# Kernel optimization log

Hardware: AMD Instinct MI355X
Metric: run time of the kernel (lower is better)

The kernel has to match this reference:

```python
import jax, jax.numpy as jnp
import numpy as np

B, S, D, A, E = 32, 2048, 512, 64, 64
EPS = 1e-5

def setup_inputs() -> dict:
    key = jax.random.key(0)
    ks = jax.random.split(key, 12)
    sc = 0.02
    return {
        "source_embedding": jax.random.normal(ks[0], (B, E), jnp.float32),
        "inputs": jax.random.normal(ks[1], (B, S, D), jnp.float32),
        "down_w_W": sc * jax.random.normal(ks[2], (E, A * D), jnp.float32),
        "down_w_b": jnp.zeros((A * D,), jnp.float32),
        "down_b_W": sc * jax.random.normal(ks[3], (E, A), jnp.float32),
        "down_b_b": jnp.zeros((A,), jnp.float32),
        "up_w_W": sc * jax.random.normal(ks[4], (E, D * A), jnp.float32),
        "up_w_b": jnp.zeros((D * A,), jnp.float32),
        "up_b_W": sc * jax.random.normal(ks[5], (E, D), jnp.float32),
        "up_b_b": jnp.zeros((D,), jnp.float32),
        "pre_w_W": sc * jax.random.normal(ks[6], (E, D), jnp.float32),
        "pre_w_b": jnp.ones((D,), jnp.float32),
        "pre_b_W": sc * jax.random.normal(ks[7], (E, D), jnp.float32),
        "pre_b_b": jnp.zeros((D,), jnp.float32),
        "post_w_W": sc * jax.random.normal(ks[8], (E, D), jnp.float32),
        "post_w_b": jnp.ones((D,), jnp.float32),
        "post_b_W": sc * jax.random.normal(ks[9], (E, D), jnp.float32),
        "post_b_b": jnp.zeros((D,), jnp.float32),
    }

def _cond_ln(x, w, b):
    # x: [B,S,D]; w,b: [B,D] -> per-sample affine layernorm over last dim
    mean = jnp.mean(x, axis=2, keepdims=True)
    var = jnp.mean((x - mean) ** 2, axis=2, keepdims=True) + EPS
    return (x - mean) / jnp.sqrt(var) * w[:, None, :] + b[:, None, :]

def reference(source_embedding, inputs,
              down_w_W, down_w_b, down_b_W, down_b_b,
              up_w_W, up_w_b, up_b_W, up_b_b,
              pre_w_W, pre_w_b, pre_b_W, pre_b_b,
              post_w_W, post_w_b, post_b_W, post_b_b):
    emb = source_embedding  # [B,E]
    # hypernet-generated per-sample adapter weights
    w_down = (emb @ down_w_W + down_w_b).reshape(B, A, D)  # [B,A,D]
    b_down = emb @ down_b_W + down_b_b                      # [B,A]
    w_up = (emb @ up_w_W + up_w_b).reshape(B, D, A)         # [B,D,A]
    b_up = emb @ up_b_W + up_b_b                            # [B,D]
    # conditional pre layernorm
    pre_w = emb @ pre_w_W + pre_w_b
    pre_b = emb @ pre_b_W + pre_b_b
    z = _cond_ln(inputs, pre_w, pre_b)
    # adapter: down-proj, relu, up-proj (matmul with weight.transpose(1,2))
    down = jnp.einsum('bsd,bad->bsa', z, w_down) + b_down[:, None, :]
    mid = jax.nn.relu(down)
    out = jnp.einsum('bsa,bda->bsd', mid, w_up) + b_up[:, None, :]
    # conditional post layernorm
    post_w = emb @ post_w_W + post_w_b
    post_b = emb @ post_b_W + post_b_b
    out = _cond_ln(out, post_w, post_b)
    return out + inputs
```

## Files before the change

kernel.cpp:

```cpp
#include <hip/hip_runtime.h>

#define NB 32
#define NS 2048
#define ND 512
#define NA 64
#define NE 64

typedef __bf16 bf16x8 __attribute__((ext_vector_type(8)));
typedef float f32x4 __attribute__((ext_vector_type(4)));

__device__ __forceinline__ unsigned short f2bf(float f) {
    union { float f; unsigned u; } v; v.f = f;
    unsigned r = (v.u + 0x7fffu + ((v.u >> 16) & 1u)) >> 16;
    return (unsigned short)r;
}
__device__ __forceinline__ unsigned pk(float a, float b) {
    return (unsigned)f2bf(a) | ((unsigned)f2bf(b) << 16);
}

#define BAR() do { asm volatile("s_waitcnt lgkmcnt(0)" ::: "memory"); \
                   __builtin_amdgcn_s_barrier(); } while (0)

__global__ __launch_bounds__(256) void hyper_vec(
    const float* __restrict__ emb,
    const float* __restrict__ pwW, const float* __restrict__ pwb,
    const float* __restrict__ pbW, const float* __restrict__ pbb,
    const float* __restrict__ powW, const float* __restrict__ powb,
    const float* __restrict__ pobW, const float* __restrict__ pobb,
    const float* __restrict__ ubW, const float* __restrict__ ubb,
    const float* __restrict__ dbW, const float* __restrict__ dbb,
    float* __restrict__ vecs) {
    int gid = blockIdx.x * 256 + threadIdx.x;
    if (gid >= NB * 2624) return;
    int b = gid / 2624;
    int r = gid - b * 2624;
    const float* W; const float* bias; int off, width;
    if (r < 2560) {
        int v = r >> 9; off = r & 511; width = 512;
        switch (v) {
            case 0:  W = pwW;  bias = pwb;  break;
            case 1:  W = pbW;  bias = pbb;  break;
            case 2:  W = powW; bias = powb; break;
            case 3:  W = pobW; bias = pobb; break;
            default: W = ubW;  bias = ubb;  break;
        }
    } else {
        off = r - 2560; width = 64; W = dbW; bias = dbb;
    }
    float acc = bias[off];
    const float* e = emb + b * 64;
#pragma unroll 8
    for (int k = 0; k < 64; ++k) acc = fmaf(e[k], W[k * width + off], acc);
    vecs[gid] = acc;
}

__global__ __launch_bounds__(256) void hyper_pack(
    const float* __restrict__ emb,
    const float* __restrict__ dwW, const float* __restrict__ dwb,
    const float* __restrict__ uwW, const float* __restrict__ uwb,
    const float* __restrict__ vecs,
    unsigned short* __restrict__ wdfrag, unsigned short* __restrict__ wufrag,
    float* __restrict__ cvec) {
    __shared__ float Wt[64][128];
    __shared__ float embs[NB * NE];
    const int tid = threadIdx.x;
    const int lane = tid & 63;
    const int bx = blockIdx.x;
    const int mat = bx >> 8;
    const int chunk = bx & 255;
    const int base = chunk * 128;
    const int colo = tid & 127;
    const int bh = tid >> 7;
    const float* W = mat ? uwW : dwW;
    const float* bias = mat ? uwb : dwb;

    for (int i = tid; i < NB * NE; i += 256) embs[i] = emb[i];
    for (int i = tid; i < 64 * 32; i += 256) {
        int k = i >> 5, c = (i & 31) << 2;
        *(float4*)&Wt[k][c] = *(const float4*)&W[(size_t)k * 32768 + base + c];
    }
    __syncthreads();

    const int col = base + colo;
    const float bv = bias[col];
    float acc[16];
#pragma unroll
    for (int b = 0; b < 16; ++b) acc[b] = bv;

    for (int k0 = 0; k0 < 64; k0 += 4) {
        float w0 = Wt[k0][colo], w1 = Wt[k0 + 1][colo];
        float w2 = Wt[k0 + 2][colo], w3 = Wt[k0 + 3][colo];
#pragma unroll
        for (int b = 0; b < 16; ++b) {
            float4 e = *(const float4*)&embs[(bh * 16 + b) * 64 + k0];
            acc[b] = fmaf(e.x, w0, acc[b]);
            acc[b] = fmaf(e.y, w1, acc[b]);
            acc[b] = fmaf(e.z, w2, acc[b]);
            acc[b] = fmaf(e.w, w3, acc[b]);
        }
    }

    if (mat == 0) {
        int a = col >> 9, d = col & 511;
        size_t idx0 = ((size_t)((a >> 4) * 16 + (d >> 5)) * 64 +
                       (((d & 31) >> 3) * 16 + (a & 15))) * 8 + (d & 7);
#pragma unroll
        for (int b = 0; b < 16; ++b) {
            int bg = bh * 16 + b;
            float raw = acc[b];
            float pw = vecs[bg * 2624 + d];
            float pb = vecs[bg * 2624 + 512 + d];
            float f = raw * pw;
            wdfrag[idx0 + (size_t)bg * 32768] = f2bf(f);
            float c2v = f, c1v = raw * pb;
#pragma unroll
            for (int m = 1; m <= 32; m <<= 1) {
                c2v += __shfl_xor(c2v, m);
                c1v += __shfl_xor(c1v, m);
            }
            if (lane == 0) {
                atomicAdd(&cvec[bg * 128 + 2 * a], c1v);
                atomicAdd(&cvec[bg * 128 + 2 * a + 1], c2v);
            }
        }
    } else {
        int d = col >> 6, a = col & 63;
        size_t idx0 = ((size_t)((d >> 4) * 2 + (a >> 5)) * 64 +
                       (((a & 31) >> 3) * 16 + (d & 15))) * 8 + (a & 7);
#pragma unroll
        for (int b = 0; b < 16; ++b)
            wufrag[idx0 + (size_t)(bh * 16 + b) * 32768] = f2bf(acc[b]);
    }
}

__global__ __launch_bounds__(256, 3) void fused_adapter(
    const float* __restrict__ inp,
    const unsigned short* __restrict__ wdfold,
    const unsigned short* __restrict__ wufrag,
    const float* __restrict__ vecs,
    const float* __restrict__ cvec,
    float* __restrict__ out) {
    __shared__ __align__(16) float x_lds[16][516];
    __shared__ __align__(16) unsigned short z_lds[16][520];
    __shared__ __align__(16) unsigned short mid_lds[16][72];
    __shared__ __align__(16) float preS[2][16][4], preQ[2][16][4];
    __shared__ __align__(16) float postS[16][4], postQ[16][4];

    const int tid = threadIdx.x;
    const int lane = tid & 63;
    const int wave = tid >> 6;
    const int lanelo = lane & 15;
    const int quad = lane >> 4;
    const int bx0 = blockIdx.x;
    const int bx = (bx0 & 7) * 128 + (bx0 >> 3);
    const int b = bx >> 5;
    const int s_base = (bx & 31) * 64;

    const float* vb = vecs + b * 2624;

    const float* xpw = inp + ((size_t)b * NS + s_base + lanelo) * ND + wave * 128 + quad * 8;
    float4 x0[4], x1[4];
#pragma unroll
    for (int kc2 = 0; kc2 < 4; ++kc2) {
        x0[kc2] = *(const float4*)(xpw + kc2 * 32);
        x1[kc2] = *(const float4*)(xpw + kc2 * 32 + 4);
    }

    float bu8[8], pw8[8], pb8[8];
#pragma unroll
    for (int i = 0; i < 8; ++i) {
        int col = (wave * 8 + i) * 16 + lanelo;
        pw8[i] = vb[1024 + col];
        pb8[i] = vb[1536 + col];
        bu8[i] = vb[2048 + col];
    }
    const unsigned short* wd = wdfold + (size_t)b * 32768;
    const unsigned short* wu = wufrag + (size_t)b * 32768;
    const int a_col = wave * 16 + lanelo;
    const float2 cc = *(const float2*)(cvec + b * 128 + 2 * a_col);
    const float c1 = cc.x + vb[2560 + a_col];

    auto stage = [&](int buf) {
        float s = 0.f, q = 0.f;
#pragma unroll
        for (int kc2 = 0; kc2 < 4; ++kc2) {
            float4 a = x0[kc2], c = x1[kc2];
            s += (a.x + a.y + a.z + a.w) + (c.x + c.y + c.z + c.w);
            q = fmaf(a.x, a.x, q); q = fmaf(a.y, a.y, q);
            q = fmaf(a.z, a.z, q); q = fmaf(a.w, a.w, q);
            q = fmaf(c.x, c.x, q); q = fmaf(c.y, c.y, q);
            q = fmaf(c.z, c.z, q); q = fmaf(c.w, c.w, q);
            uint4 au;
            au.x = pk(a.x, a.y); au.y = pk(a.z, a.w);
            au.z = pk(c.x, c.y); au.w = pk(c.z, c.w);
            int col = wave * 128 + kc2 * 32 + quad * 8;
            *(uint4*)&z_lds[lanelo][col] = au;
            *(float4*)&x_lds[lanelo][col] = a;
            *(float4*)&x_lds[lanelo][col + 4] = c;
        }
        s += __shfl_xor(s, 16); s += __shfl_xor(s, 32);
        q += __shfl_xor(q, 16); q += __shfl_xor(q, 32);
        if (lane < 16) { preS[buf][lane][wave] = s; preQ[buf][lane][wave] = q; }
    };
    auto loadx = [&](const float* p) {
#pragma unroll
        for (int kc2 = 0; kc2 < 4; ++kc2) {
            x0[kc2] = *(const float4*)(p + kc2 * 32);
            x1[kc2] = *(const float4*)(p + kc2 * 32 + 4);
        }
    };

    stage(0);
    loadx(xpw + 16 * ND);
    BAR();

    for (int t = 0; t < 4; ++t) {
        float rs[4], mrs[4];
#pragma unroll
        for (int r = 0; r < 4; ++r) {
            int row = quad * 4 + r;
            float4 S = *(const float4*)preS[t & 1][row];
            float4 Q = *(const float4*)preQ[t & 1][row];
            float ss = (S.x + S.y) + (S.z + S.w);
            float qq = (Q.x + Q.y) + (Q.z + Q.w);
            float mean = ss * (1.0f / 512.0f);
            float var = qq * (1.0f / 512.0f) - mean * mean;
            float rstd = rsqrtf(var + 1e-5f);
            rs[r] = rstd;
            mrs[r] = mean * rstd;
        }

        f32x4 accd = (f32x4){0.f, 0.f, 0.f, 0.f};
#pragma unroll
        for (int kc = 0; kc < 16; ++kc) {
            uint4 azu = *(const uint4*)&z_lds[lanelo][kc * 32 + quad * 8];
            uint4 bv = *(const uint4*)(wd + ((size_t)(wave * 16 + kc) * 64 + lane) * 8);
            accd = __builtin_amdgcn_mfma_f32_16x16x32_bf16(
                __builtin_bit_cast(bf16x8, azu), __builtin_bit_cast(bf16x8, bv), accd, 0, 0, 0);
        }
#pragma unroll
        for (int r = 0; r < 4; ++r) {
            float v = fmaf(rs[r], accd[r], fmaf(-mrs[r], cc.y, c1));
            mid_lds[quad * 4 + r][a_col] = f2bf(fmaxf(v, 0.0f));
        }
        BAR();

        uint4 a0u = *(const uint4*)&mid_lds[lanelo][quad * 8];
        uint4 a1u = *(const uint4*)&mid_lds[lanelo][32 + quad * 8];
        bf16x8 af0 = __builtin_bit_cast(bf16x8, a0u);
        bf16x8 af1 = __builtin_bit_cast(bf16x8, a1u);
        f32x4 acc8[8];
        float sum[4] = {0.f, 0.f, 0.f, 0.f}, sq[4] = {0.f, 0.f, 0.f, 0.f};
#pragma unroll
        for (int nt8 = 0; nt8 < 8; ++nt8) {
            int nt = wave * 8 + nt8;
            uint4 b0 = *(const uint4*)(wu + ((size_t)(nt * 2 + 0) * 64 + lane) * 8);
            uint4 b1 = *(const uint4*)(wu + ((size_t)(nt * 2 + 1) * 64 + lane) * 8);
            f32x4 a4 = (f32x4){0.f, 0.f, 0.f, 0.f};
            a4 = __builtin_amdgcn_mfma_f32_16x16x32_bf16(af0, __builtin_bit_cast(bf16x8, b0), a4, 0, 0, 0);
            a4 = __builtin_amdgcn_mfma_f32_16x16x32_bf16(af1, __builtin_bit_cast(bf16x8, b1), a4, 0, 0, 0);
            float buv = bu8[nt8];
#pragma unroll
            for (int r = 0; r < 4; ++r) {
                float y = a4[r] + buv;
                a4[r] = y;
                sum[r] += y;
                sq[r] = fmaf(y, y, sq[r]);
            }
            acc8[nt8] = a4;
        }
#pragma unroll
        for (int r = 0; r < 4; ++r) {
#pragma unroll
            for (int m = 1; m <= 8; m <<= 1) {
                sum[r] += __shfl_xor(sum[r], m);
                sq[r] += __shfl_xor(sq[r], m);
            }
        }
        if (lanelo == 0) {
#pragma unroll
            for (int r = 0; r < 4; ++r) {
                postS[quad * 4 + r][wave] = sum[r];
                postQ[quad * 4 + r][wave] = sq[r];
            }
        }
        BAR();

        float mean2[4], rstd2[4];
#pragma unroll
        for (int r = 0; r < 4; ++r) {
            int row = quad * 4 + r;
            float4 S = *(const float4*)postS[row];
            float4 Q = *(const float4*)postQ[row];
            float ss = (S.x + S.y) + (S.z + S.w);
            float qq = (Q.x + Q.y) + (Q.z + Q.w);
            mean2[r] = ss * (1.0f / 512.0f);
            float v2 = qq * (1.0f / 512.0f) - mean2[r] * mean2[r];
            rstd2[r] = rsqrtf(v2 + 1e-5f);
        }

        const size_t obase = ((size_t)b * NS + s_base + t * 16) * ND;
#pragma unroll
        for (int nt8 = 0; nt8 < 8; ++nt8) {
            int col = (wave * 8 + nt8) * 16 + lanelo;
#pragma unroll
            for (int r = 0; r < 4; ++r) {
                size_t off = obase + (size_t)(quad * 4 + r) * ND + col;
                float xres = x_lds[quad * 4 + r][col];
                out[off] = fmaf((acc8[nt8][r] - mean2[r]) * rstd2[r],
                                pw8[nt8], pb8[nt8]) + xres;
            }
        }
        BAR();

        if (t < 3) {
            stage((t + 1) & 1);
            if (t < 2) loadx(xpw + (size_t)(t + 2) * 16 * ND);
            BAR();
        }
    }
}

extern "C" void kernel_launch(void* const* d_in, const int* in_sizes, int n_in,
                              void* d_out, int out_size, void* d_ws, size_t ws_size,
                              hipStream_t stream) {
    const float* emb  = (const float*)d_in[0];
    const float* inp  = (const float*)d_in[1];
    const float* dwW  = (const float*)d_in[2];
    const float* dwb  = (const float*)d_in[3];
    const float* dbW  = (const float*)d_in[4];
    const float* dbb  = (const float*)d_in[5];
    const float* uwW  = (const float*)d_in[6];
    const float* uwb  = (const float*)d_in[7];
    const float* ubW  = (const float*)d_in[8];
    const float* ubb  = (const float*)d_in[9];
    const float* pwW  = (const float*)d_in[10];
    const float* pwb  = (const float*)d_in[11];
    const float* pbW  = (const float*)d_in[12];
    const float* pbb  = (const float*)d_in[13];
    const float* powW = (const float*)d_in[14];
    const float* powb = (const float*)d_in[15];
    const float* pobW = (const float*)d_in[16];
    const float* pobb = (const float*)d_in[17];

    unsigned short* wdfrag = (unsigned short*)d_ws;
    unsigned short* wufrag = wdfrag + (size_t)NB * 32768;
    float* vecs = (float*)(wufrag + (size_t)NB * 32768);
    float* cvec = vecs + (size_t)NB * 2624;

    hyper_vec<<<(NB * 2624 + 255) / 256, 256, 0, stream>>>(
        emb, pwW, pwb, pbW, pbb, powW, powb, pobW, pobb, ubW, ubb, dbW, dbb, vecs);
    hipMemsetAsync(cvec, 0, (size_t)NB * 128 * sizeof(float), stream);
    hyper_pack<<<512, 256, 0, stream>>>(emb, dwW, dwb, uwW, uwb, vecs,
                                        wdfrag, wufrag, cvec);
    fused_adapter<<<NB * (NS / 64), 256, 0, stream>>>(
        inp, wdfrag, wufrag, vecs, cvec, (float*)d_out);
}
```

Before: 393.0 us.

## Stream input tiles into LDS via async global_load_lds double buffering

```diff
diff --git a/kernel.cpp b/kernel.cpp
--- a/kernel.cpp
+++ b/kernel.cpp
@@ -7,6 +7,7 @@
 #define NE 64
 
 typedef __bf16 bf16x8 __attribute__((ext_vector_type(8)));
+typedef __bf16 bf16x2 __attribute__((ext_vector_type(2)));
 typedef float f32x4 __attribute__((ext_vector_type(4)));
 
 __device__ __forceinline__ unsigned short f2bf(float f) {
@@ -14,12 +15,18 @@
     unsigned r = (v.u + 0x7fffu + ((v.u >> 16) & 1u)) >> 16;
     return (unsigned short)r;
 }
-__device__ __forceinline__ unsigned pk(float a, float b) {
-    return (unsigned)f2bf(a) | ((unsigned)f2bf(b) << 16);
+__device__ __forceinline__ unsigned pk2(float lo, float hi) {
+    bf16x2 t; t[0] = (__bf16)lo; t[1] = (__bf16)hi;
+    return __builtin_bit_cast(unsigned, t);
+}
+__device__ __forceinline__ unsigned short f2bfn(float f) {
+    __bf16 h = (__bf16)f; return __builtin_bit_cast(unsigned short, h);
 }
 
 #define BAR() do { asm volatile("s_waitcnt lgkmcnt(0)" ::: "memory"); \
                    __builtin_amdgcn_s_barrier(); } while (0)
+#define BARVM() do { asm volatile("s_waitcnt vmcnt(0) lgkmcnt(0)" ::: "memory"); \
+                     __builtin_amdgcn_s_barrier(); } while (0)
 
 __global__ __launch_bounds__(256) void hyper_vec(
     const float* __restrict__ emb,
@@ -133,17 +140,16 @@
     }
 }
 
-__global__ __launch_bounds__(256, 3) void fused_adapter(
+__global__ __launch_bounds__(256, 2) void fused_adapter(
     const float* __restrict__ inp,
     const unsigned short* __restrict__ wdfold,
     const unsigned short* __restrict__ wufrag,
     const float* __restrict__ vecs,
     const float* __restrict__ cvec,
     float* __restrict__ out) {
-    __shared__ __align__(16) float x_lds[16][516];
-    __shared__ __align__(16) unsigned short z_lds[16][520];
+    __shared__ __align__(16) float x0_lds[16 * 516];
+    __shared__ __align__(16) float x1_lds[16 * 516];
     __shared__ __align__(16) unsigned short mid_lds[16][72];
-    __shared__ __align__(16) float preS[2][16][4], preQ[2][16][4];
     __shared__ __align__(16) float postS[16][4], postQ[16][4];
 
     const int tid = threadIdx.x;
@@ -152,21 +158,33 @@
     const int lanelo = lane & 15;
     const int quad = lane >> 4;
     const int bx0 = blockIdx.x;
-    const int bx = (bx0 & 7) * 128 + (bx0 >> 3);
-    const int b = bx >> 5;
-    const int s_base = (bx & 31) * 64;
+    const int bx = (bx0 & 7) * 64 + (bx0 >> 3);
+    const int b = bx >> 4;
+    const int sgrp = (bx & 15) * 128;
 
     const float* vb = vecs + b * 2624;
-
-    const float* xpw = inp + ((size_t)b * NS + s_base + lanelo) * ND + wave * 128 + quad * 8;
-    float4 x0[4], x1[4];
-#pragma unroll
-    for (int kc2 = 0; kc2 < 4; ++kc2) {
-        x0[kc2] = *(const float4*)(xpw + kc2 * 32);
-        x1[kc2] = *(const float4*)(xpw + kc2 * 32 + 4);
-    }
-
-    float bu8[8], pw8[8], pb8[8];
+    const unsigned short* wd = wdfold + (size_t)b * 32768;
+    const unsigned short* wu = wufrag + (size_t)b * 32768;
+
+    auto dma = [&](int t, float* xb) {
+        const float* src = inp + ((size_t)b * NS + sgrp + t * 16 + wave * 4) * ND
+                           + lane * 4;
+        float* dst = xb + (wave * 4) * 516;
+#pragma unroll
+        for (int rr = 0; rr < 4; ++rr) {
+#pragma unroll
+            for (int h = 0; h < 2; ++h) {
+                __builtin_amdgcn_global_load_lds(
+                    (const __attribute__((address_space(1))) void*)(src + rr * ND + h * 256),
+                    (__attribute__((address_space(3))) void*)(dst + rr * 516 + h * 256),
+                    16, 0, 0);
+            }
+        }
+    };
+
+    dma(0, x0_lds);
+    dma(1, x1_lds);
+    float pw8[8], pb8[8], bu8[8];
 #pragma unroll
     for (int i = 0; i < 8; ++i) {
         int col = (wave * 8 + i) * 16 + lanelo;
@@ -174,74 +192,44 @@
         pb8[i] = vb[1536 + col];
         bu8[i] = vb[2048 + col];
     }
-    const unsigned short* wd = wdfold + (size_t)b * 32768;
-    const unsigned short* wu = wufrag + (size_t)b * 32768;
     const int a_col = wave * 16 + lanelo;
     const float2 cc = *(const float2*)(cvec + b * 128 + 2 * a_col);
     const float c1 = cc.x + vb[2560 + a_col];
-
-    auto stage = [&](int buf) {
+    asm volatile("s_waitcnt vmcnt(0)" ::: "memory");
+    __builtin_amdgcn_s_barrier();
+
+    auto tile = [&](int t, float* xc) {
         float s = 0.f, q = 0.f;
-#pragma unroll
-        for (int kc2 = 0; kc2 < 4; ++kc2) {
-            float4 a = x0[kc2], c = x1[kc2];
-            s += (a.x + a.y + a.z + a.w) + (c.x + c.y + c.z + c.w);
-            q = fmaf(a.x, a.x, q); q = fmaf(a.y, a.y, q);
-            q = fmaf(a.z, a.z, q); q = fmaf(a.w, a.w, q);
-            q = fmaf(c.x, c.x, q); q = fmaf(c.y, c.y, q);
-            q = fmaf(c.z, c.z, q); q = fmaf(c.w, c.w, q);
+        f32x4 accd = (f32x4){0.f, 0.f, 0.f, 0.f};
+#pragma unroll
+        for (int kc = 0; kc < 16; ++kc) {
+            const float* xr = xc + lanelo * 516 + kc * 32 + quad * 8;
+            f32x4 xa = *(const f32x4*)xr;
+            f32x4 xb = *(const f32x4*)(xr + 4);
+            s += (xa[0] + xa[1]) + (xa[2] + xa[3]) + (xb[0] + xb[1]) + (xb[2] + xb[3]);
+            q = fmaf(xa[0], xa[0], q); q = fmaf(xa[1], xa[1], q);
+            q = fmaf(xa[2], xa[2], q); q = fmaf(xa[3], xa[3], q);
+            q = fmaf(xb[0], xb[0], q); q = fmaf(xb[1], xb[1], q);
+            q = fmaf(xb[2], xb[2], q); q = fmaf(xb[3], xb[3], q);
             uint4 au;
-            au.x = pk(a.x, a.y); au.y = pk(a.z, a.w);
-            au.z = pk(c.x, c.y); au.w = pk(c.z, c.w);
-            int col = wave * 128 + kc2 * 32 + quad * 8;
-            *(uint4*)&z_lds[lanelo][col] = au;
-            *(float4*)&x_lds[lanelo][col] = a;
-            *(float4*)&x_lds[lanelo][col + 4] = c;
+            au.x = pk2(xa[0], xa[1]); au.y = pk2(xa[2], xa[3]);
+            au.z = pk2(xb[0], xb[1]); au.w = pk2(xb[2], xb[3]);
+            uint4 bv = *(const uint4*)(wd + ((size_t)(wave * 16 + kc) * 64 + lane) * 8);
+            accd = __builtin_amdgcn_mfma_f32_16x16x32_bf16(
+                __builtin_bit_cast(bf16x8, au), __builtin_bit_cast(bf16x8, bv), accd, 0, 0, 0);
         }
         s += __shfl_xor(s, 16); s += __shfl_xor(s, 32);
         q += __shfl_xor(q, 16); q += __shfl_xor(q, 32);
-        if (lane < 16) { preS[buf][lane][wave] = s; preQ[buf][lane][wave] = q; }
-    };
-    auto loadx = [&](const float* p) {
-#pragma unroll
-        for (int kc2 = 0; kc2 < 4; ++kc2) {
-            x0[kc2] = *(const float4*)(p + kc2 * 32);
-            x1[kc2] = *(const float4*)(p + kc2 * 32 + 4);
-        }
-    };
-
-    stage(0);
-    loadx(xpw + 16 * ND);
-    BAR();
-
-    for (int t = 0; t < 4; ++t) {
-        float rs[4], mrs[4];
+        float mean = s * (1.0f / 512.0f);
+        float var = q * (1.0f / 512.0f) - mean * mean;
+        float rstd = rsqrtf(var + 1e-5f);
+        float mrsl = mean * rstd;
 #pragma unroll
         for (int r = 0; r < 4; ++r) {
-            int row = quad * 4 + r;
-            float4 S = *(const float4*)preS[t & 1][row];
-            float4 Q = *(const float4*)preQ[t & 1][row];
-            float ss = (S.x + S.y) + (S.z + S.w);
-            float qq = (Q.x + Q.y) + (Q.z + Q.w);
-            float mean = ss * (1.0f / 512.0f);
-            float var = qq * (1.0f / 512.0f) - mean * mean;
-            float rstd = rsqrtf(var + 1e-5f);
-            rs[r] = rstd;
-            mrs[r] = mean * rstd;
-        }
-
-        f32x4 accd = (f32x4){0.f, 0.f, 0.f, 0.f};
-#pragma unroll
-        for (int kc = 0; kc < 16; ++kc) {
-            uint4 azu = *(const uint4*)&z_lds[lanelo][kc * 32 + quad * 8];
-            uint4 bv = *(const uint4*)(wd + ((size_t)(wave * 16 + kc) * 64 + lane) * 8);
-            accd = __builtin_amdgcn_mfma_f32_16x16x32_bf16(
-                __builtin_bit_cast(bf16x8, azu), __builtin_bit_cast(bf16x8, bv), accd, 0, 0, 0);
-        }
-#pragma unroll
-        for (int r = 0; r < 4; ++r) {
-            float v = fmaf(rs[r], accd[r], fmaf(-mrs[r], cc.y, c1));
-            mid_lds[quad * 4 + r][a_col] = f2bf(fmaxf(v, 0.0f));
+            float rsr = __shfl(rstd, quad * 4 + r);
+            float mrr = __shfl(mrsl, quad * 4 + r);
+            float v = fmaf(rsr, accd[r], fmaf(-mrr, cc.y, c1));
+            mid_lds[quad * 4 + r][a_col] = f2bfn(fmaxf(v, 0.0f));
         }
         BAR();
 
@@ -299,25 +287,26 @@
             rstd2[r] = rsqrtf(v2 + 1e-5f);
         }
 
-        const size_t obase = ((size_t)b * NS + s_base + t * 16) * ND;
+        const size_t obase = ((size_t)b * NS + sgrp + t * 16) * ND;
 #pragma unroll
         for (int nt8 = 0; nt8 < 8; ++nt8) {
             int col = (wave * 8 + nt8) * 16 + lanelo;
 #pragma unroll
             for (int r = 0; r < 4; ++r) {
                 size_t off = obase + (size_t)(quad * 4 + r) * ND + col;
-                float xres = x_lds[quad * 4 + r][col];
+                float xres = xc[(quad * 4 + r) * 516 + col];
                 out[off] = fmaf((acc8[nt8][r] - mean2[r]) * rstd2[r],
                                 pw8[nt8], pb8[nt8]) + xres;
             }
         }
-        BAR();
-
-        if (t < 3) {
-            stage((t + 1) & 1);
-            if (t < 2) loadx(xpw + (size_t)(t + 2) * 16 * ND);
-            BAR();
-        }
+        BARVM();
+        if (t < 6) dma(t + 2, xc);
+    };
+
+#pragma unroll 1
+    for (int tt = 0; tt < 8; tt += 2) {
+        tile(tt, x0_lds);
+        tile(tt + 1, x1_lds);
     }
 }
 
@@ -353,6 +342,6 @@
     hipMemsetAsync(cvec, 0, (size_t)NB * 128 * sizeof(float), stream);
     hyper_pack<<<512, 256, 0, stream>>>(emb, dwW, dwb, uwW, uwb, vecs,
                                         wdfrag, wufrag, cvec);
-    fused_adapter<<<NB * (NS / 64), 256, 0, stream>>>(
+    fused_adapter<<<512, 256, 0, stream>>>(
         inp, wdfrag, wufrag, vecs, cvec, (float*)d_out);
 }
```

Result: faster. 364.1 us (-7.4%).
